# Performance work log

Measured on AMD Instinct MI355X. Metric: run time of the kernel, lower is better.

## Reference

```python
import jax, jax.numpy as jnp
import numpy as np

N = 100000   # nodes
E = 1600000  # edges
G = 512      # graphs
ATOM = 64
HID = 64
CLS = 10


def layer_norm(x, g, b, eps=1e-5):
    mu = jnp.mean(x, axis=-1, keepdims=True)
    var = jnp.mean((x - mu) ** 2, axis=-1, keepdims=True)
    return (x - mu) * jax.lax.rsqrt(var + eps) * g + b


def gcn_conv(x, src, dst, W, b, fill, num_nodes):
    # PyG GCNConv with add_self_loops: A_hat = A + fill*I, sym-normalized.
    h = x @ W                                            # [N, F_out]
    ones = jnp.ones(src.shape[0], dtype=h.dtype)
    deg = jax.ops.segment_sum(ones, dst, num_segments=num_nodes) + fill
    dinv = jax.lax.rsqrt(deg)                            # deg^{-1/2}
    norm = dinv[src] * dinv[dst]                         # [E]
    msg = h[src] * norm[:, None]                         # gather + scale
    out = jax.ops.segment_sum(msg, dst, num_segments=num_nodes)
    out = out + (fill * dinv * dinv)[:, None] * h        # self-loop term
    return out + b


def setup_inputs() -> dict:
    key = jax.random.key(0)
    ks = jax.random.split(key, 8)
    x = jax.random.normal(ks[0], (N, ATOM), dtype=jnp.float32)
    edge_index = jax.random.randint(ks[1], (2, E), 0, N, dtype=jnp.int64)
    batch = jnp.sort(jax.random.randint(ks[2], (N,), 0, G, dtype=jnp.int64))
    s = lambda k, sh, fan: jax.random.normal(k, sh, jnp.float32) / np.sqrt(fan)
    return {
        "x": x, "edge_index": edge_index, "batch": batch,
        "W1": s(ks[3], (ATOM, HID), ATOM), "b1": jnp.zeros((HID,), jnp.float32),
        "ln_g": jnp.ones((HID,), jnp.float32), "ln_b": jnp.zeros((HID,), jnp.float32),
        "W2": s(ks[4], (HID, HID), HID), "b2": jnp.zeros((HID,), jnp.float32),
        "W3": s(ks[5], (HID, 768), HID), "b3": jnp.zeros((768,), jnp.float32),
        "ln2_g": jnp.ones((768,), jnp.float32), "ln2_b": jnp.zeros((768,), jnp.float32),
        "W4": s(ks[6], (768, CLS), 768), "b4": jnp.zeros((CLS,), jnp.float32),
    }


def reference(x, edge_index, batch, W1, b1, ln_g, ln_b, W2, b2,
              W3, b3, ln2_g, ln2_b, W4, b4):
    src, dst = edge_index[0], edge_index[1]
    leaky = lambda v: jax.nn.leaky_relu(v, 0.2)
    # GCN1 (improved=True -> self-loop weight 2.0) + LN + LeakyReLU
    h = gcn_conv(x, src, dst, W1, b1, 2.0, N)
    h = leaky(layer_norm(h, ln_g, ln_b))
    # GCN2 (self-loop weight 1.0) + LeakyReLU
    h = gcn_conv(h, src, dst, W2, b2, 1.0, N)
    h = leaky(h)
    # global max pool over graphs
    pooled = jax.ops.segment_max(h, batch, num_segments=G)  # [G, HID]
    # seq2 head (Dropout is identity at inference)
    z = pooled @ W3 + b3
    z = leaky(layer_norm(z, ln2_g, ln2_b))
    z = z @ W4 + b4
    return jax.nn.softmax(z, axis=-1)
```

## Files before the change

kernel.cpp:

```cpp
#include <hip/hip_runtime.h>
#include <hip/hip_bf16.h>

#define NODES 100000
#define EDGES 1600000
#define NGRAPH 512
#define BINROWS 512
#define NBINS 196
#define BINCAP 12288
#define CHUNK 4096
#define NCHUNKS ((EDGES + CHUNK - 1) / CHUNK)
#define VSS 72

using bf16 = __hip_bfloat16;
typedef long long ll;
using frag8 = __attribute__((ext_vector_type(8))) short;
using f32x4 = __attribute__((ext_vector_type(4))) float;

__device__ __forceinline__ float lrelu(float v) { return v > 0.0f ? v : 0.2f * v; }

__device__ __forceinline__ unsigned mapf(float f) {
    unsigned u = __float_as_uint(f);
    return (u & 0x80000000u) ? ~u : (u | 0x80000000u);
}
__device__ __forceinline__ float unmapf(unsigned u) {
    return __uint_as_float((u & 0x80000000u) ? (u ^ 0x80000000u) : ~u);
}

__device__ __forceinline__ int idx_at(const void* raw, int i, int f) {
    return f ? (int)((const ll*)raw)[i] : ((const int*)raw)[i];
}

__device__ __forceinline__ unsigned short tobf(float f) {
    bf16 h = __float2bfloat16(f);
    return *reinterpret_cast<unsigned short*>(&h);
}

__global__ void sentinel_kernel(float* out, float v) {
    int i = blockIdx.x * blockDim.x + threadIdx.x;
    if (i < NGRAPH * 10) out[i] = v;
}

__global__ void binPlace(const int* __restrict__ eiw, int* __restrict__ flag,
                         int* __restrict__ binCursor, unsigned* __restrict__ staging) {
    __shared__ unsigned recs[CHUNK];
    __shared__ unsigned char binsA[CHUNK];
    __shared__ int hist[NBINS], lstart[NBINS + 1], baseg[NBINS], lcur[NBINS];
    __shared__ int red[4];
    int t = threadIdx.x;
    int e0 = blockIdx.x * CHUNK;
    int eEnd = min(e0 + CHUNK, EDGES);
    int v = 0;
    for (int k = e0 + t; k < eEnd; k += 256) v |= eiw[2 * k + 1];
    for (int o = 32; o; o >>= 1) v |= __shfl_xor(v, o);
    if ((t & 63) == 0) red[t >> 6] = v;
    if (t < NBINS) { hist[t] = 0; lcur[t] = 0; }
    __syncthreads();
    int f = ((red[0] | red[1] | red[2] | red[3]) == 0) ? 1 : 0;
    if (blockIdx.x == 0 && t == 0) flag[0] = f;
    const void* ei = (const void*)eiw;
    for (int i = e0 + t; i < eEnd; i += 256) {
        int s = idx_at(ei, i, f), d = idx_at(ei, EDGES + i, f);
        if ((unsigned)s < NODES && (unsigned)d < NODES) atomicAdd(&hist[d >> 9], 1);
    }
    __syncthreads();
    if (t == 0) {
        int acc = 0;
        for (int bb = 0; bb < NBINS; ++bb) {
            lstart[bb] = acc;
            acc += hist[bb];
        }
        lstart[NBINS] = acc;
    }
    __syncthreads();
    if (t < NBINS && hist[t] > 0) baseg[t] = atomicAdd(&binCursor[t], hist[t]);
    __syncthreads();
    for (int i = e0 + t; i < eEnd; i += 256) {
        int s = idx_at(ei, i, f), d = idx_at(ei, EDGES + i, f);
        if ((unsigned)s < NODES && (unsigned)d < NODES) {
            int bb = d >> 9;
            int p = lstart[bb] + atomicAdd(&lcur[bb], 1);
            recs[p] = ((unsigned)s << 9) | (unsigned)(d & 511);
            binsA[p] = (unsigned char)bb;
        }
    }
    __syncthreads();
    int nv = lstart[NBINS];
    for (int p = t; p < nv; p += 256) {
        int bb = binsA[p];
        int idx = baseg[bb] + (p - lstart[bb]);
        if (idx < BINCAP) staging[(size_t)bb * BINCAP + idx] = recs[p];
    }
}

__global__ void csr_finalize(const unsigned* __restrict__ staging,
                             const int* __restrict__ binCursor, int* __restrict__ row_ptr,
                             float* __restrict__ dinv1, float* __restrict__ dinv2,
                             int* __restrict__ csr_src) {
    __shared__ int lhist[BINROWS];
    __shared__ int sc[256];
    __shared__ int startSh;
    int b = blockIdx.x, t = threadIdx.x;
    int cv = (t < NBINS) ? binCursor[t] : 0;
    sc[t] = (t < b) ? cv : 0;
    __syncthreads();
    for (int o = 128; o; o >>= 1) {
        if (t < o) sc[t] += sc[t + o];
        __syncthreads();
    }
    if (t == 0) startSh = sc[0];
    __syncthreads();
    int myStart = startSh;
    int cnt = binCursor[b];
    if (b == NBINS - 1 && t == 0) row_ptr[NODES] = myStart + cnt;
    const unsigned* st = staging + (size_t)b * BINCAP;
    int r0 = b << 9;
    for (int j = t; j < BINROWS; j += 256) lhist[j] = 0;
    __syncthreads();
    for (int p = t; p < cnt; p += 256) atomicAdd(&lhist[st[p] & 511], 1);
    __syncthreads();
    int base = t * 2;
    int v0 = lhist[base], v1 = lhist[base + 1];
    int tsum = v0 + v1;
    sc[t] = tsum;
    __syncthreads();
    for (int o = 1; o < 256; o <<= 1) {
        int u = (t >= o) ? sc[t - o] : 0;
        __syncthreads();
        sc[t] += u;
        __syncthreads();
    }
    int excl = sc[t] - tsum;
    int ex0 = excl, ex1 = excl + v0;
#pragma unroll
    for (int k = 0; k < 2; ++k) {
        int row = r0 + base + k;
        int ex = k ? ex1 : ex0;
        int dgz = k ? v1 : v0;
        if (row < NODES) {
            row_ptr[row] = myStart + ex;
            float dg = (float)dgz;
            dinv1[row] = 1.0f / sqrtf(dg + 2.0f);
            dinv2[row] = 1.0f / sqrtf(dg + 1.0f);
        }
    }
    __syncthreads();
    lhist[base] = ex0;
    lhist[base + 1] = ex1;
    __syncthreads();
    for (int p = t; p < cnt; p += 256) {
        unsigned rec = st[p];
        int slot = atomicAdd(&lhist[rec & 511], 1);
        csr_src[myStart + slot] = (int)(rec >> 9);
    }
}

__global__ void prescale_x(const float* __restrict__ x, const float* __restrict__ dinv1,
                           bf16* __restrict__ xs) {
    int i = blockIdx.x * blockDim.x + threadIdx.x;
    if (i >= NODES * 16) return;
    int row = i >> 4;
    float4 xv = ((const float4*)x)[i];
    float d1 = dinv1[row];
    uint2 p;
    p.x = (unsigned)tobf(xv.x * d1) | ((unsigned)tobf(xv.y * d1) << 16);
    p.y = (unsigned)tobf(xv.z * d1) | ((unsigned)tobf(xv.w * d1) << 16);
    ((uint2*)xs)[i] = p;
}

__device__ __forceinline__ void gather_quad2(
    const uint2* __restrict__ feat4, const int* __restrict__ csr, int begA, int endA,
    int begB, int endB, int lane, float& oxA, float& oyA, float& ozA, float& owA,
    float& oxB, float& oyB, float& ozB, float& owB) {
    int q = lane >> 4, c = lane & 15;
    float a1x = 0, a1y = 0, a1z = 0, a1w = 0, a2x = 0, a2y = 0, a2z = 0, a2w = 0;
    float b1x = 0, b1y = 0, b1z = 0, b1w = 0, b2x = 0, b2y = 0, b2z = 0, b2w = 0;
    int cbA = begA, cbB = begB;
    while (cbA < endA || cbB < endB) {
        int cntA = endA - cbA;
        cntA = cntA > 64 ? 64 : (cntA < 0 ? 0 : cntA);
        int cntB = endB - cbB;
        cntB = cntB > 64 ? 64 : (cntB < 0 ? 0 : cntB);
        int idxA = (lane < cntA) ? csr[cbA + lane] : 0;
        int idxB = (lane < cntB) ? csr[cbB + lane] : 0;
        int jm = cntA > cntB ? cntA : cntB;
        for (int j = 0; j < jm; j += 8) {
            int e0 = j + q, e1 = j + 4 + q;
            if (j < cntA) {
                int sA0 = __shfl(idxA, e0);
                uint2 uA0 = feat4[(size_t)sA0 * 16 + c];
                if (e0 < cntA) {
                    a1x += __uint_as_float(uA0.x << 16);
                    a1y += __uint_as_float(uA0.x & 0xffff0000u);
                    a1z += __uint_as_float(uA0.y << 16);
                    a1w += __uint_as_float(uA0.y & 0xffff0000u);
                }
                if (j + 4 < cntA) {
                    int sA1 = __shfl(idxA, e1);
                    uint2 uA1 = feat4[(size_t)sA1 * 16 + c];
                    if (e1 < cntA) {
                        a2x += __uint_as_float(uA1.x << 16);
                        a2y += __uint_as_float(uA1.x & 0xffff0000u);
                        a2z += __uint_as_float(uA1.y << 16);
                        a2w += __uint_as_float(uA1.y & 0xffff0000u);
                    }
                }
            }
            if (j < cntB) {
                int sB0 = __shfl(idxB, e0);
                uint2 uB0 = feat4[(size_t)sB0 * 16 + c];
                if (e0 < cntB) {
                    b1x += __uint_as_float(uB0.x << 16);
                    b1y += __uint_as_float(uB0.x & 0xffff0000u);
                    b1z += __uint_as_float(uB0.y << 16);
                    b1w += __uint_as_float(uB0.y & 0xffff0000u);
                }
                if (j + 4 < cntB) {
                    int sB1 = __shfl(idxB, e1);
                    uint2 uB1 = feat4[(size_t)sB1 * 16 + c];
                    if (e1 < cntB) {
                        b2x += __uint_as_float(uB1.x << 16);
                        b2y += __uint_as_float(uB1.x & 0xffff0000u);
                        b2z += __uint_as_float(uB1.y << 16);
                        b2w += __uint_as_float(uB1.y & 0xffff0000u);
                    }
                }
            }
        }
        cbA += 64;
        cbB += 64;
    }
    a1x += a2x; a1y += a2y; a1z += a2z; a1w += a2w;
    b1x += b2x; b1y += b2y; b1z += b2z; b1w += b2w;
    a1x += __shfl_xor(a1x, 16); a1y += __shfl_xor(a1y, 16);
    a1z += __shfl_xor(a1z, 16); a1w += __shfl_xor(a1w, 16);
    b1x += __shfl_xor(b1x, 16); b1y += __shfl_xor(b1y, 16);
    b1z += __shfl_xor(b1z, 16); b1w += __shfl_xor(b1w, 16);
    a1x += __shfl_xor(a1x, 32); a1y += __shfl_xor(a1y, 32);
    a1z += __shfl_xor(a1z, 32); a1w += __shfl_xor(a1w, 32);
    b1x += __shfl_xor(b1x, 32); b1y += __shfl_xor(b1y, 32);
    b1z += __shfl_xor(b1z, 32); b1w += __shfl_xor(b1w, 32);
    oxA = a1x; oyA = a1y; ozA = a1z; owA = a1w;
    oxB = b1x; oyB = b1y; ozB = b1z; owB = b1w;
}

__device__ __forceinline__ void gcn_core(const uint2* __restrict__ feat4,
                                         const int* __restrict__ csr,
                                         const int* __restrict__ rp,
                                         const float* __restrict__ dinv, float selfw,
                                         const float* __restrict__ W, short* Vs, short* Wt,
                                         int rowBase, int lane, int wave, f32x4 (&acc)[4]) {
    int t = wave * 64 + lane;
    for (int i = t; i < 4096; i += 256) {
        int k = i >> 6, n = i & 63;
        Wt[n * VSS + k] = (short)tobf(W[i]);
    }
    __syncthreads();
    int myBase = rowBase + wave * 16;
    int rpv = (lane < 17) ? rp[min(myBase + lane, NODES)] : 0;
    int c = lane & 15;
    for (int ii = 0; ii < 8; ++ii) {
        int iA = ii, iB = ii + 8;
        int begA = __shfl(rpv, iA), endA = __shfl(rpv, iA + 1);
        int begB = __shfl(rpv, iB), endB = __shfl(rpv, iB + 1);
        float vxA, vyA, vzA, vwA, vxB, vyB, vzB, vwB;
        gather_quad2(feat4, csr, begA, endA, begB, endB, lane, vxA, vyA, vzA, vwA, vxB,
                     vyB, vzB, vwB);
        int rowA = myBase + iA, rowB = myBase + iB;
        float dvA = 0.0f, dvB = 0.0f;
        uint2 usA = make_uint2(0u, 0u), usB = make_uint2(0u, 0u);
        if (rowA < NODES) {
            dvA = dinv[rowA];
            usA = feat4[(size_t)rowA * 16 + c];
        }
        if (rowB < NODES) {
            dvB = dinv[rowB];
            usB = feat4[(size_t)rowB * 16 + c];
        }
        vxA = dvA * (vxA + selfw * __uint_as_float(usA.x << 16));
        vyA = dvA * (vyA + selfw * __uint_as_float(usA.x & 0xffff0000u));
        vzA = dvA * (vzA + selfw * __uint_as_float(usA.y << 16));
        vwA = dvA * (vwA + selfw * __uint_as_float(usA.y & 0xffff0000u));
        vxB = dvB * (vxB + selfw * __uint_as_float(usB.x << 16));
        vyB = dvB * (vyB + selfw * __uint_as_float(usB.x & 0xffff0000u));
        vzB = dvB * (vzB + selfw * __uint_as_float(usB.y << 16));
        vwB = dvB * (vwB + selfw * __uint_as_float(usB.y & 0xffff0000u));
        if (lane < 16) {
            uint2 pA, pB;
            pA.x = (unsigned)tobf(vxA) | ((unsigned)tobf(vyA) << 16);
            pA.y = (unsigned)tobf(vzA) | ((unsigned)tobf(vwA) << 16);
            pB.x = (unsigned)tobf(vxB) | ((unsigned)tobf(vyB) << 16);
            pB.y = (unsigned)tobf(vzB) | ((unsigned)tobf(vwB) << 16);
            *(uint2*)(Vs + (size_t)(wave * 16 + iA) * VSS + c * 4) = pA;
            *(uint2*)(Vs + (size_t)(wave * 16 + iB) * VSS + c * 4) = pB;
        }
    }
    frag8 afr[2];
    int m = lane & 15, q = lane >> 4;
#pragma unroll
    for (int ks = 0; ks < 2; ++ks)
        afr[ks] = *(frag8*)(Vs + (size_t)(wave * 16 + m) * VSS + q * 8 + ks * 32);
#pragma unroll
    for (int nt = 0; nt < 4; ++nt) {
        f32x4 a = {0.f, 0.f, 0.f, 0.f};
#pragma unroll
        for (int ks = 0; ks < 2; ++ks) {
            frag8 bfr = *(frag8*)(Wt + (size_t)(nt * 16 + m) * VSS + q * 8 + ks * 32);
            a = __builtin_amdgcn_mfma_f32_16x16x32_bf16(afr[ks], bfr, a, 0, 0, 0);
        }
        acc[nt] = a;
    }
}

__global__ void __launch_bounds__(256, 2)
gcn1_fused(const uint2* __restrict__ xs4, const int* __restrict__ csr,
           const int* __restrict__ rp, const float* __restrict__ dinv1,
           const float* __restrict__ dinv2, const float* __restrict__ W1,
           const float* __restrict__ b1, const float* __restrict__ lng,
           const float* __restrict__ lnb, bf16* __restrict__ h1s) {
    __shared__ short sm[2 * 64 * VSS];
    short* Vs = sm;
    short* Wt = sm + 64 * VSS;
    int lane = threadIdx.x & 63, wave = threadIdx.x >> 6;
    int rowBase = blockIdx.x * 64;
    f32x4 acc[4];
    gcn_core(xs4, csr, rp, dinv1, 2.0f, W1, Vs, Wt, rowBase, lane, wave, acc);
    int c = lane & 15, q = lane >> 4;
    float bc[4], lg[4], lb[4];
#pragma unroll
    for (int nt = 0; nt < 4; ++nt) {
        bc[nt] = b1[nt * 16 + c];
        lg[nt] = lng[nt * 16 + c];
        lb[nt] = lnb[nt * 16 + c];
    }
#pragma unroll
    for (int r = 0; r < 4; ++r) {
        int grow = rowBase + wave * 16 + q * 4 + r;
        float v0 = acc[0][r] + bc[0], v1 = acc[1][r] + bc[1];
        float v2 = acc[2][r] + bc[2], v3 = acc[3][r] + bc[3];
        float s = v0 + v1 + v2 + v3;
        for (int o = 1; o < 16; o <<= 1) s += __shfl_xor(s, o);
        float mu = s * (1.0f / 64.0f);
        float d0 = v0 - mu, d1 = v1 - mu, d2 = v2 - mu, d3 = v3 - mu;
        float qq = d0 * d0 + d1 * d1 + d2 * d2 + d3 * d3;
        for (int o = 1; o < 16; o <<= 1) qq += __shfl_xor(qq, o);
        float rstd = 1.0f / sqrtf(qq * (1.0f / 64.0f) + 1e-5f);
        if (grow < NODES) {
            float d2v = dinv2[grow];
            bf16* dst = h1s + (size_t)grow * 64 + c;
            dst[0]  = __float2bfloat16(lrelu(d0 * rstd * lg[0] + lb[0]) * d2v);
            dst[16] = __float2bfloat16(lrelu(d1 * rstd * lg[1] + lb[1]) * d2v);
            dst[32] = __float2bfloat16(lrelu(d2 * rstd * lg[2] + lb[2]) * d2v);
            dst[48] = __float2bfloat16(lrelu(d3 * rstd * lg[3] + lb[3]) * d2v);
        }
    }
}

__global__ void __launch_bounds__(256, 2)
gcn2_fused(const uint2* __restrict__ h1s4, const int* __restrict__ csr,
           const int* __restrict__ rp, const float* __restrict__ dinv2,
           const float* __restrict__ W2, const float* __restrict__ b2,
           const void* __restrict__ batch, const int* __restrict__ flag,
           unsigned* __restrict__ pooled) {
    __shared__ short sm[2 * 64 * VSS];
    __shared__ int gsh[64];
    short* Vs = sm;
    short* Wt = sm + 64 * VSS;
    int t = threadIdx.x, lane = t & 63, wave = t >> 6;
    int rowBase = blockIdx.x * 64;
    if (t < 64) {
        int row = rowBase + t;
        gsh[t] = (row < NODES) ? idx_at(batch, row, flag[0]) : -1;
    }
    f32x4 acc[4];
    gcn_core(h1s4, csr, rp, dinv2, 1.0f, W2, Vs, Wt, rowBase, lane, wave, acc);
    int c = lane & 15, q = lane >> 4;
    float bc[4];
#pragma unroll
    for (int nt = 0; nt < 4; ++nt) bc[nt] = b2[nt * 16 + c];
    __syncthreads();
    float* P = (float*)sm;
#pragma unroll
    for (int r = 0; r < 4; ++r) {
        int mloc = wave * 16 + q * 4 + r;
#pragma unroll
        for (int nt = 0; nt < 4; ++nt)
            P[(size_t)mloc * 65 + nt * 16 + c] = lrelu(acc[nt][r] + bc[nt]);
    }
    __syncthreads();
    if (wave == 0) {
        float m = P[lane];
        int gc = gsh[0];
        for (int r = 1; r < 64; ++r) {
            int gr = gsh[r];
            float ar = P[(size_t)r * 65 + lane];
            if (gr == gc) {
                m = fmaxf(m, ar);
            } else {
                if ((unsigned)gc < NGRAPH) atomicMax(&pooled[gc * 64 + lane], mapf(m));
                gc = gr;
                m = ar;
            }
        }
        if ((unsigned)gc < NGRAPH) atomicMax(&pooled[gc * 64 + lane], mapf(m));
    }
}

__global__ void head_kernel(const unsigned* __restrict__ pooled, const float* __restrict__ W3,
                            const float* __restrict__ b3, const float* __restrict__ g2,
                            const float* __restrict__ be2, const float* __restrict__ W4,
                            const float* __restrict__ b4, float* __restrict__ out) {
    __shared__ float prow[64];
    __shared__ float z[768];
    __shared__ float rs[4], rss[4];
    __shared__ float mu_s, rstd_s;
    __shared__ float red[10];
    int t = threadIdx.x, gI = blockIdx.x;
    if (t < 64) prow[t] = unmapf(pooled[gI * 64 + t]);
    __syncthreads();
    for (int c = t; c < 768; c += 256) {
        float acc = b3[c];
#pragma unroll 16
        for (int k = 0; k < 64; ++k) acc += prow[k] * W3[k * 768 + c];
        z[c] = acc;
    }
    __syncthreads();
    float s = 0.0f, ss = 0.0f;
    for (int c = t; c < 768; c += 256) {
        float v = z[c];
        s += v;
        ss += v * v;
    }
    for (int o = 32; o; o >>= 1) {
        s += __shfl_xor(s, o);
        ss += __shfl_xor(ss, o);
    }
    if ((t & 63) == 0) { rs[t >> 6] = s; rss[t >> 6] = ss; }
    __syncthreads();
    if (t == 0) {
        float S = rs[0] + rs[1] + rs[2] + rs[3];
        float SS = rss[0] + rss[1] + rss[2] + rss[3];
        float mu = S * (1.0f / 768.0f);
        float var = SS * (1.0f / 768.0f) - mu * mu;
        mu_s = mu;
        rstd_s = 1.0f / sqrtf(fmaxf(var, 0.0f) + 1e-5f);
    }
    __syncthreads();
    for (int c = t; c < 768; c += 256) {
        float y = (z[c] - mu_s) * rstd_s * g2[c] + be2[c];
        z[c] = lrelu(y);
    }
    if (t < 10) red[t] = 0.0f;
    __syncthreads();
    float p[10];
#pragma unroll
    for (int c = 0; c < 10; ++c) p[c] = 0.0f;
    for (int k = t; k < 768; k += 256) {
        float zv = z[k];
#pragma unroll
        for (int c = 0; c < 10; ++c) p[c] += zv * W4[k * 10 + c];
    }
#pragma unroll
    for (int c = 0; c < 10; ++c) atomicAdd(&red[c], p[c]);
    __syncthreads();
    if (t == 0) {
        float l[10], m = -1e30f;
#pragma unroll
        for (int c = 0; c < 10; ++c) {
            l[c] = red[c] + b4[c];
            m = fmaxf(m, l[c]);
        }
        float sum = 0.0f;
#pragma unroll
        for (int c = 0; c < 10; ++c) {
            l[c] = expf(l[c] - m);
            sum += l[c];
        }
        float inv = 1.0f / sum;
#pragma unroll
        for (int c = 0; c < 10; ++c) out[gI * 10 + c] = l[c] * inv;
    }
}

extern "C" void kernel_launch(void* const* d_in, const int* in_sizes, int n_in,
                              void* d_out, int out_size, void* d_ws, size_t ws_size,
                              hipStream_t stream) {
    const size_t REQUIRED = (size_t)NODES * 64 * 2 * 2
                          + (size_t)EDGES * 4
                          + (size_t)(NODES + 1) * 4
                          + (size_t)NODES * 4 * 2
                          + (size_t)NBINS * 4
                          + (size_t)NGRAPH * 64 * 4
                          + 16;
    if (ws_size < REQUIRED) {
        sentinel_kernel<<<20, 256, 0, stream>>>((float*)d_out, 64.0f);
        return;
    }

    const float* x = (const float*)d_in[0];
    const int* eiw = (const int*)d_in[1];
    const void* batch = d_in[2];
    const float* W1 = (const float*)d_in[3];
    const float* b1 = (const float*)d_in[4];
    const float* lng = (const float*)d_in[5];
    const float* lnb = (const float*)d_in[6];
    const float* W2 = (const float*)d_in[7];
    const float* b2 = (const float*)d_in[8];
    const float* W3 = (const float*)d_in[9];
    const float* b3 = (const float*)d_in[10];
    const float* g2 = (const float*)d_in[11];
    const float* be2 = (const float*)d_in[12];
    const float* W4 = (const float*)d_in[13];
    const float* b4 = (const float*)d_in[14];

    bf16* xs = (bf16*)d_ws;
    bf16* h1s = xs + (size_t)NODES * 64;
    unsigned* staging = (unsigned*)h1s;
    int* csr_src = (int*)(h1s + (size_t)NODES * 64);
    int* row_ptr = csr_src + EDGES;
    float* dinv1 = (float*)(row_ptr + NODES + 1);
    float* dinv2 = dinv1 + NODES;
    int* binCursor = (int*)(dinv2 + NODES);
    unsigned* pooled = (unsigned*)(binCursor + NBINS);
    int* flag = (int*)(pooled + NGRAPH * 64);

    hipMemsetAsync(binCursor, 0, (size_t)NBINS * 4, stream);
    hipMemsetAsync(pooled, 0, (size_t)NGRAPH * 64 * 4, stream);

    binPlace<<<NCHUNKS, 256, 0, stream>>>(eiw, flag, binCursor, staging);
    csr_finalize<<<NBINS, 256, 0, stream>>>(staging, binCursor, row_ptr, dinv1, dinv2,
                                            csr_src);
    prescale_x<<<(NODES * 16 + 255) / 256, 256, 0, stream>>>(x, dinv1, xs);

    gcn1_fused<<<(NODES + 63) / 64, 256, 0, stream>>>((const uint2*)xs, csr_src, row_ptr,
                                                      dinv1, dinv2, W1, b1, lng, lnb, h1s);
    gcn2_fused<<<(NODES + 63) / 64, 256, 0, stream>>>((const uint2*)h1s, csr_src, row_ptr,
                                                      dinv2, W2, b2, batch, flag, pooled);

    head_kernel<<<NGRAPH, 256, 0, stream>>>(pooled, W3, b3, g2, be2, W4, b4, (float*)d_out);
}
```

Baseline: 305.7 us.

## Replace binned CSR build with global-atomic degree count, scan, and scatter

Replaces the two-pass, shared-memory binned CSR construction (binPlace and csr_finalize with a staging buffer) with three simpler kernels. The new kernels do a per-node degree count using global atomics, a per-block prefix scan over degrees to produce row_ptr, cursors and dinv, and an edge scatter that uses a global atomic cursor per destination. The aim is to drop the staging buffer and the in-shared sorting work. In exchange it issues two rounds of random global atomics over all edges, and each scan block re-sums every earlier degree. Edge order within each row also becomes nondeterministic.

```diff
diff --git a/kernel.cpp b/kernel.cpp
--- a/kernel.cpp
+++ b/kernel.cpp
@@ -6,7 +6,6 @@
 #define NGRAPH 512
 #define BINROWS 512
 #define NBINS 196
-#define BINCAP 12288
 #define CHUNK 4096
 #define NCHUNKS ((EDGES + CHUNK - 1) / CHUNK)
 #define VSS 72
@@ -40,11 +39,8 @@
     if (i < NGRAPH * 10) out[i] = v;
 }
 
-__global__ void binPlace(const int* __restrict__ eiw, int* __restrict__ flag,
-                         int* __restrict__ binCursor, unsigned* __restrict__ staging) {
-    __shared__ unsigned recs[CHUNK];
-    __shared__ unsigned char binsA[CHUNK];
-    __shared__ int hist[NBINS], lstart[NBINS + 1], baseg[NBINS], lcur[NBINS];
+__global__ void deg_count(const int* __restrict__ eiw, int* __restrict__ flag,
+                          int* __restrict__ deg) {
     __shared__ int red[4];
     int t = threadIdx.x;
     int e0 = blockIdx.x * CHUNK;
@@ -53,55 +49,26 @@
     for (int k = e0 + t; k < eEnd; k += 256) v |= eiw[2 * k + 1];
     for (int o = 32; o; o >>= 1) v |= __shfl_xor(v, o);
     if ((t & 63) == 0) red[t >> 6] = v;
-    if (t < NBINS) { hist[t] = 0; lcur[t] = 0; }
     __syncthreads();
     int f = ((red[0] | red[1] | red[2] | red[3]) == 0) ? 1 : 0;
     if (blockIdx.x == 0 && t == 0) flag[0] = f;
     const void* ei = (const void*)eiw;
     for (int i = e0 + t; i < eEnd; i += 256) {
         int s = idx_at(ei, i, f), d = idx_at(ei, EDGES + i, f);
-        if ((unsigned)s < NODES && (unsigned)d < NODES) atomicAdd(&hist[d >> 9], 1);
-    }
-    __syncthreads();
-    if (t == 0) {
-        int acc = 0;
-        for (int bb = 0; bb < NBINS; ++bb) {
-            lstart[bb] = acc;
-            acc += hist[bb];
-        }
-        lstart[NBINS] = acc;
-    }
-    __syncthreads();
-    if (t < NBINS && hist[t] > 0) baseg[t] = atomicAdd(&binCursor[t], hist[t]);
-    __syncthreads();
-    for (int i = e0 + t; i < eEnd; i += 256) {
-        int s = idx_at(ei, i, f), d = idx_at(ei, EDGES + i, f);
-        if ((unsigned)s < NODES && (unsigned)d < NODES) {
-            int bb = d >> 9;
-            int p = lstart[bb] + atomicAdd(&lcur[bb], 1);
-            recs[p] = ((unsigned)s << 9) | (unsigned)(d & 511);
-            binsA[p] = (unsigned char)bb;
-        }
-    }
-    __syncthreads();
-    int nv = lstart[NBINS];
-    for (int p = t; p < nv; p += 256) {
-        int bb = binsA[p];
-        int idx = baseg[bb] + (p - lstart[bb]);
-        if (idx < BINCAP) staging[(size_t)bb * BINCAP + idx] = recs[p];
-    }
-}
-
-__global__ void csr_finalize(const unsigned* __restrict__ staging,
-                             const int* __restrict__ binCursor, int* __restrict__ row_ptr,
-                             float* __restrict__ dinv1, float* __restrict__ dinv2,
-                             int* __restrict__ csr_src) {
-    __shared__ int lhist[BINROWS];
+        if ((unsigned)s < NODES && (unsigned)d < NODES) atomicAdd(&deg[d], 1);
+    }
+}
+
+__global__ void row_scan(const int* __restrict__ deg, int* __restrict__ row_ptr,
+                         float* __restrict__ dinv1, float* __restrict__ dinv2,
+                         int* __restrict__ cursor) {
     __shared__ int sc[256];
     __shared__ int startSh;
     int b = blockIdx.x, t = threadIdx.x;
-    int cv = (t < NBINS) ? binCursor[t] : 0;
-    sc[t] = (t < b) ? cv : 0;
+    int r0 = b << 9;
+    int pre = 0;
+    for (int i = t; i < r0; i += 256) pre += deg[i];
+    sc[t] = pre;
     __syncthreads();
     for (int o = 128; o; o >>= 1) {
         if (t < o) sc[t] += sc[t + o];
@@ -110,16 +77,11 @@
     if (t == 0) startSh = sc[0];
     __syncthreads();
     int myStart = startSh;
-    int cnt = binCursor[b];
-    if (b == NBINS - 1 && t == 0) row_ptr[NODES] = myStart + cnt;
-    const unsigned* st = staging + (size_t)b * BINCAP;
-    int r0 = b << 9;
-    for (int j = t; j < BINROWS; j += 256) lhist[j] = 0;
-    __syncthreads();
-    for (int p = t; p < cnt; p += 256) atomicAdd(&lhist[st[p] & 511], 1);
     __syncthreads();
     int base = t * 2;
-    int v0 = lhist[base], v1 = lhist[base + 1];
+    int row0 = r0 + base, row1 = row0 + 1;
+    int v0 = (row0 < NODES) ? deg[row0] : 0;
+    int v1 = (row1 < NODES) ? deg[row1] : 0;
     int tsum = v0 + v1;
     sc[t] = tsum;
     __syncthreads();
@@ -133,24 +95,34 @@
     int ex0 = excl, ex1 = excl + v0;
 #pragma unroll
     for (int k = 0; k < 2; ++k) {
-        int row = r0 + base + k;
+        int row = k ? row1 : row0;
         int ex = k ? ex1 : ex0;
         int dgz = k ? v1 : v0;
         if (row < NODES) {
-            row_ptr[row] = myStart + ex;
+            int rstart = myStart + ex;
+            row_ptr[row] = rstart;
+            cursor[row] = rstart;
             float dg = (float)dgz;
             dinv1[row] = 1.0f / sqrtf(dg + 2.0f);
             dinv2[row] = 1.0f / sqrtf(dg + 1.0f);
         }
     }
-    __syncthreads();
-    lhist[base] = ex0;
-    lhist[base + 1] = ex1;
-    __syncthreads();
-    for (int p = t; p < cnt; p += 256) {
-        unsigned rec = st[p];
-        int slot = atomicAdd(&lhist[rec & 511], 1);
-        csr_src[myStart + slot] = (int)(rec >> 9);
+    if (b == NBINS - 1 && t == 255) row_ptr[NODES] = myStart + sc[255];
+}
+
+__global__ void edge_scatter(const int* __restrict__ eiw, const int* __restrict__ flag,
+                             int* __restrict__ cursor, int* __restrict__ csr_src) {
+    int t = threadIdx.x;
+    int e0 = blockIdx.x * CHUNK;
+    int eEnd = min(e0 + CHUNK, EDGES);
+    int f = flag[0];
+    const void* ei = (const void*)eiw;
+    for (int i = e0 + t; i < eEnd; i += 256) {
+        int s = idx_at(ei, i, f), d = idx_at(ei, EDGES + i, f);
+        if ((unsigned)s < NODES && (unsigned)d < NODES) {
+            int slot = atomicAdd(&cursor[d], 1);
+            csr_src[slot] = s;
+        }
     }
 }
 
@@ -488,7 +460,6 @@
                           + (size_t)EDGES * 4
                           + (size_t)(NODES + 1) * 4
                           + (size_t)NODES * 4 * 2
-                          + (size_t)NBINS * 4
                           + (size_t)NGRAPH * 64 * 4
                           + 16;
     if (ws_size < REQUIRED) {
@@ -514,21 +485,21 @@
 
     bf16* xs = (bf16*)d_ws;
     bf16* h1s = xs + (size_t)NODES * 64;
-    unsigned* staging = (unsigned*)h1s;
+    int* cursor = (int*)h1s;
     int* csr_src = (int*)(h1s + (size_t)NODES * 64);
+    int* deg = csr_src;
     int* row_ptr = csr_src + EDGES;
     float* dinv1 = (float*)(row_ptr + NODES + 1);
     float* dinv2 = dinv1 + NODES;
-    int* binCursor = (int*)(dinv2 + NODES);
-    unsigned* pooled = (unsigned*)(binCursor + NBINS);
+    unsigned* pooled = (unsigned*)(dinv2 + NODES);
     int* flag = (int*)(pooled + NGRAPH * 64);
 
-    hipMemsetAsync(binCursor, 0, (size_t)NBINS * 4, stream);
+    hipMemsetAsync(deg, 0, (size_t)NODES * 4, stream);
     hipMemsetAsync(pooled, 0, (size_t)NGRAPH * 64 * 4, stream);
 
-    binPlace<<<NCHUNKS, 256, 0, stream>>>(eiw, flag, binCursor, staging);
-    csr_finalize<<<NBINS, 256, 0, stream>>>(staging, binCursor, row_ptr, dinv1, dinv2,
-                                            csr_src);
+    deg_count<<<NCHUNKS, 256, 0, stream>>>(eiw, flag, deg);
+    row_scan<<<NBINS, 256, 0, stream>>>(deg, row_ptr, dinv1, dinv2, cursor);
+    edge_scatter<<<NCHUNKS, 256, 0, stream>>>(eiw, flag, cursor, csr_src);
     prescale_x<<<(NODES * 16 + 255) / 256, 256, 0, stream>>>(x, dinv1, xs);
 
     gcn1_fused<<<(NODES + 63) / 64, 256, 0, stream>>>((const uint2*)xs, csr_src, row_ptr,
```

After: 466.2 us. 1.53x slower.
